# Optimization experiments

Hardware: AMD Instinct MI355X
Metric: run time of the kernel (lower is better)

The kernel has to match this reference:

```python
import jax, jax.numpy as jnp
import numpy as np

DIM = 256; N_HEADS = 8; HEAD_DIM = DIM // N_HEADS
RELU_DIM = 1024; LN_DIM = 512; N_LN = 2; EMB_DIM = 256
VOCAB = 32000; N_CLASSES = 16; B = 8; SEQ = 256
N_ITERS = 12   # fixed-point iterations of the DEQ solve (ITFn2)
EPS = 1e-5     # torch LayerNorm default eps


def sinusoidal_pos_emb(T, d):
    pos = np.arange(T)[:, None].astype(np.float32)
    i = np.arange(d // 2)[None, :].astype(np.float32)
    ang = pos / np.power(10000.0, 2.0 * i / d)
    pe = np.zeros((T, d), np.float32)
    pe[:, 0::2] = np.sin(ang)
    pe[:, 1::2] = np.cos(ang)
    return jnp.asarray(pe)


def setup_inputs() -> dict:
    key = jax.random.key(0)
    ks = jax.random.split(key, 8)
    x = jax.random.randint(ks[0], (B, SEQ), 0, VOCAB)
    seq_lens = jax.random.randint(ks[1], (B,), 1, SEQ + 1)
    emb = jax.random.normal(ks[2], (VOCAB + 1, EMB_DIM), jnp.float32) * EMB_DIM ** -0.5
    emb = emb.at[VOCAB].set(0.0)  # padding_idx row
    cls_token = jax.random.normal(ks[3], (1, 1, EMB_DIM), jnp.float32) * EMB_DIM ** -0.5
    # scaled down vs kaiming so the fixed-point map is contractive (module enforces this via project())
    A = jax.random.normal(ks[4], (RELU_DIM + LN_DIM, RELU_DIM + LN_DIM + DIM + EMB_DIM), jnp.float32) * 0.01
    b = jnp.zeros((RELU_DIM + LN_DIM,), jnp.float32)
    A_qkv = jax.random.normal(ks[5], (3 * DIM, LN_DIM), jnp.float32) * (2.0 / LN_DIM) ** 0.5
    W_cls = jax.random.normal(ks[6], (N_CLASSES, RELU_DIM + LN_DIM + DIM), jnp.float32) * (RELU_DIM + LN_DIM + DIM) ** -0.5
    b_cls = jnp.zeros((N_CLASSES,), jnp.float32)
    return {"x": x, "seq_lens": seq_lens, "emb": emb, "cls_token": cls_token,
            "A": A, "A_qkv": A_qkv, "b": b, "W_cls": W_cls, "b_cls": b_cls}


def reference(x, seq_lens, emb, cls_token, A, A_qkv, b, W_cls, b_cls):
    Bsz, T = x.shape
    Tp = T + 1
    # input injection: embed + sinusoidal pos, then prepend cls token
    u = emb[x] + sinusoidal_pos_emb(T, EMB_DIM)[None]
    u = jnp.concatenate([jnp.broadcast_to(cls_token, (Bsz, 1, EMB_DIM)), u], axis=1)  # (B, T+1, E)
    pos = jnp.arange(Tp)
    src_mask = (seq_lens[:, None] + 1) <= pos[None]  # (B, T+1), True = padded key
    # A_qkv rows ordered (n_heads, 3, head_dim) per scale_by_S rearrange
    Wqkv = A_qkv.reshape(N_HEADS, 3, HEAD_DIM, LN_DIM)
    scale = 1.0 / jnp.sqrt(jnp.asarray(HEAD_DIM, u.dtype))
    neg = jnp.asarray(-1e9, u.dtype)

    def step(z, _):
        # pre-activations for relu + layernorm blocks
        pre = jnp.einsum('btj,ij->bti', jnp.concatenate([z, u], axis=-1), A) + b
        z_r = jax.nn.relu(pre[..., :RELU_DIM])
        zl = pre[..., RELU_DIM:].reshape(Bsz, Tp, N_LN, LN_DIM // N_LN)
        mu = zl.mean(-1, keepdims=True)
        var = zl.var(-1, keepdims=True)
        z_l = ((zl - mu) * jax.lax.rsqrt(var + EPS)).reshape(Bsz, Tp, LN_DIM)
        # multi-head attention driven by the layernorm block
        qkv = jnp.einsum('btj,hmdj->bthmd', z_l, Wqkv)  # (B, T+1, H, 3, hd)
        q, k, v = qkv[..., 0, :], qkv[..., 1, :], qkv[..., 2, :]
        scores = jnp.einsum('bqhd,bkhd->bhqk', q, k) * scale
        scores = jnp.where(src_mask[:, None, None, :], neg, scores)
        attn = jax.nn.softmax(scores, axis=-1)
        z_a = jnp.einsum('bhqk,bkhd->bqhd', attn, v).reshape(Bsz, Tp, DIM)
        return jnp.concatenate([z_r, z_l, z_a], axis=-1), None

    z0 = jnp.zeros((Bsz, Tp, RELU_DIM + LN_DIM + DIM), u.dtype)
    z, _ = jax.lax.scan(step, z0, None, length=N_ITERS)
    # classify from the equilibrium cls-token state
    return z[:, 0] @ W_cls.T + b_cls
```

## Files before the change

kernel.cpp:

```cpp
#include <hip/hip_runtime.h>
#include <hip/hip_bf16.h>
#include <math.h>

#define TP 257
#define ROWS 2056
#define XDIM 2048
#define ZDIM 1792
#define PREDIM 1536
#define QKVDIM 768
#define EMBD 256

using f32x4  = __attribute__((ext_vector_type(4))) float;
using bf16x8 = __attribute__((ext_vector_type(8))) short;

__device__ __forceinline__ ushort f2bf(float f) {
    uint32_t u = __float_as_uint(f);
    return (ushort)((u + 0x7fffu + ((u >> 16) & 1u)) >> 16);
}
__device__ __forceinline__ float bf2f(ushort u) {
    return __uint_as_float(((uint32_t)u) << 16);
}

#define GLD16(g, l) __builtin_amdgcn_global_load_lds( \
    (const __attribute__((address_space(1))) void*)(g), \
    (__attribute__((address_space(3))) void*)(l), 16, 0, 0)

__global__ __launch_bounds__(256) void f2bf_kernel(
    const float* __restrict__ in, ushort* __restrict__ out, int n)
{
    int i = blockIdx.x * 256 + threadIdx.x;
    if (i < n) out[i] = f2bf(in[i]);
}

__global__ __launch_bounds__(256) void build_u_kernel(
    const int* __restrict__ x, const float* __restrict__ emb,
    const float* __restrict__ cls, ushort* __restrict__ xbA, ushort* __restrict__ xbB)
{
    int row = blockIdx.x;
    int e   = threadIdx.x;
    int b = row / TP, t = row % TP;
    float val;
    if (t == 0) {
        val = cls[e];
    } else {
        int tt = t - 1;
        int xi = x[b * 256 + tt];
        float ang = (float)tt * expf(-(float)(e & ~1) * 0.035978672652993f);
        float pe  = (e & 1) ? cosf(ang) : sinf(ang);
        val = emb[(size_t)xi * EMBD + e] + pe;
    }
    ushort bv = f2bf(val);
    xbA[(size_t)row * XDIM + 1792 + e] = bv;
    xbB[(size_t)row * XDIM + 1792 + e] = bv;
}

__global__ __launch_bounds__(256) void gemm_bf16_kernel(
    const ushort* __restrict__ X, int ldx,
    const ushort* __restrict__ W,
    const float* __restrict__ bias,
    float* __restrict__ C, ushort* __restrict__ Cb,
    int ldc, int M, int N, int K)
{
    __shared__ ushort As[128 * 32];
    __shared__ ushort Bs[128 * 32];
    int tid  = threadIdx.x;
    int lane = tid & 63, wv = tid >> 6;
    int wr = wv >> 1, wc = wv & 1;
    int r0 = blockIdx.x * 128, c0 = blockIdx.y * 128;

    f32x4 acc[4][4] = {};

    int srow = wv * 32 + (lane >> 2);
    int skol = (lane & 3) * 8;
    int fk   = (lane >> 4) * 8;

    for (int k0 = 0; k0 < K; k0 += 32) {
        #pragma unroll
        for (int i = 0; i < 2; ++i) {
            int rr = r0 + srow + i * 16;
            if (rr >= M) rr = M - 1;
            const ushort* ga = X + (size_t)rr * ldx + k0 + skol;
            GLD16(ga, &As[(wv * 32 + i * 16) * 32]);
            const ushort* gb = W + (size_t)(c0 + srow + i * 16) * K + k0 + skol;
            GLD16(gb, &Bs[(wv * 32 + i * 16) * 32]);
        }
        __syncthreads();

        bf16x8 a[4], b[4];
        #pragma unroll
        for (int m = 0; m < 4; ++m)
            a[m] = *(const bf16x8*)&As[(wr * 64 + m * 16 + (lane & 15)) * 32 + fk];
        #pragma unroll
        for (int n = 0; n < 4; ++n)
            b[n] = *(const bf16x8*)&Bs[(wc * 64 + n * 16 + (lane & 15)) * 32 + fk];
        #pragma unroll
        for (int m = 0; m < 4; ++m)
            #pragma unroll
            for (int n = 0; n < 4; ++n)
                acc[m][n] = __builtin_amdgcn_mfma_f32_16x16x32_bf16(a[m], b[n], acc[m][n], 0, 0, 0);
        __syncthreads();
    }

    int crow = (lane >> 4) * 4;
    int ccol = lane & 15;
    #pragma unroll
    for (int m = 0; m < 4; ++m) {
        #pragma unroll
        for (int j = 0; j < 4; ++j) {
            int r = r0 + wr * 64 + m * 16 + crow + j;
            if (r < M) {
                #pragma unroll
                for (int n = 0; n < 4; ++n) {
                    int cc = n * 16 + ccol;
                    float vb = bias ? bias[c0 + wc * 64 + cc] : 0.0f;
                    float v = acc[m][n][j] + vb;
                    if (Cb) Cb[(size_t)r * ldc + c0 + wc * 64 + cc] = f2bf(v);
                    else    C [(size_t)r * ldc + c0 + wc * 64 + cc] = v;
                }
            }
        }
    }
}

__global__ __launch_bounds__(256) void relu_ln_kernel(
    const float* __restrict__ pre, ushort* __restrict__ zb)
{
    int row = blockIdx.x;
    int tid = threadIdx.x;
    const float* pr = pre + (size_t)row * PREDIM;
    ushort* zr = zb + (size_t)row * XDIM;

    #pragma unroll
    for (int i = 0; i < 4; ++i) {
        int c = tid + i * 256;
        float v = pr[c];
        zr[c] = f2bf(v > 0.f ? v : 0.f);
    }

    __shared__ float warr[4][2];
    #pragma unroll
    for (int g = 0; g < 2; ++g) {
        float xv = pr[1024 + g * 256 + tid];
        float s = xv, s2 = xv * xv;
        #pragma unroll
        for (int off = 32; off; off >>= 1) {
            s  += __shfl_down(s, off);
            s2 += __shfl_down(s2, off);
        }
        int wave = tid >> 6, lane = tid & 63;
        if (lane == 0) { warr[wave][0] = s; warr[wave][1] = s2; }
        __syncthreads();
        float ts  = warr[0][0] + warr[1][0] + warr[2][0] + warr[3][0];
        float ts2 = warr[0][1] + warr[1][1] + warr[2][1] + warr[3][1];
        float mu  = ts * (1.0f / 256.0f);
        float var = ts2 * (1.0f / 256.0f) - mu * mu;
        float y = (xv - mu) * rsqrtf(var + 1e-5f);
        zr[1024 + g * 256 + tid] = f2bf(y);
        __syncthreads();
    }
}

__global__ __launch_bounds__(256) void attn_kernel(
    const ushort* __restrict__ qkvb, const int* __restrict__ seq_lens,
    ushort* __restrict__ zb)
{
    __shared__ ushort Kl[288 * 40];
    __shared__ ushort VTl[32 * 296];
    __shared__ ushort Pl[4][16 * 40];

    int bh = blockIdx.x;
    int b = bh >> 3, h = bh & 7;
    int kend = seq_lens[b] + 1; if (kend > TP) kend = TP;
    int tid = threadIdx.x;
    const size_t qbase = (size_t)(b * TP) * QKVDIM + h * 96;

    for (int idx = tid; idx < 31 * 32; idx += 256) {
        int row = 257 + (idx >> 5), d = idx & 31;
        Kl[row * 40 + d] = 0;
    }
    for (int idx = tid; idx < 32 * 32; idx += 256) {
        int d = idx >> 5, col = 257 + (idx & 31);
        VTl[d * 296 + col] = 0;
    }
    for (int idx = tid; idx < 257 * 4; idx += 256) {
        int row = idx >> 2, seg = idx & 3;
        *(bf16x8*)&Kl[row * 40 + seg * 8] =
            *(const bf16x8*)&qkvb[qbase + (size_t)row * QKVDIM + 32 + seg * 8];
    }
    for (int idx = tid; idx < 257 * 32; idx += 256) {
        int key = idx >> 5, d = idx & 31;
        VTl[d * 296 + key] = qkvb[qbase + (size_t)key * QKVDIM + 64 + d];
    }
    __syncthreads();

    int wave = tid >> 6, lane = tid & 63;
    int q0 = blockIdx.y * 64 + wave * 16;
    if (q0 > 256) return;
    int qcol = lane & 15, g = lane >> 4;
    int ktmax = (kend + 15) >> 4;
    const float scale = 0.17677669529663687f;

    int qg = q0 + qcol; if (qg > 256) qg = 256;
    bf16x8 aq = *(const bf16x8*)&qkvb[qbase + (size_t)qg * QKVDIM + g * 8];

    f32x4 s[17];
    const f32x4 zz = {};
    #pragma unroll
    for (int kt = 0; kt < 17; ++kt) {
        s[kt] = (f32x4)(-1e30f);
        if (kt < ktmax) {
            bf16x8 bk = *(const bf16x8*)&Kl[(kt * 16 + qcol) * 40 + g * 8];
            f32x4 r = __builtin_amdgcn_mfma_f32_16x16x32_bf16(aq, bk, zz, 0, 0, 0);
            bool kv = (kt * 16 + qcol) < kend;
            #pragma unroll
            for (int j = 0; j < 4; ++j)
                s[kt][j] = kv ? r[j] * scale : -1e30f;
        }
    }

    float m0[4], l0[4];
    #pragma unroll
    for (int j = 0; j < 4; ++j) m0[j] = -3.0e38f;
    #pragma unroll
    for (int kt = 0; kt < 17; ++kt)
        #pragma unroll
        for (int j = 0; j < 4; ++j) m0[j] = fmaxf(m0[j], s[kt][j]);
    #pragma unroll
    for (int j = 0; j < 4; ++j) {
        #pragma unroll
        for (int off = 1; off < 16; off <<= 1)
            m0[j] = fmaxf(m0[j], __shfl_xor(m0[j], off));
        l0[j] = 0.f;
    }
    #pragma unroll
    for (int kt = 0; kt < 17; ++kt)
        #pragma unroll
        for (int j = 0; j < 4; ++j) {
            float p = __expf(s[kt][j] - m0[j]);
            s[kt][j] = p;
            l0[j] += p;
        }
    #pragma unroll
    for (int j = 0; j < 4; ++j) {
        #pragma unroll
        for (int off = 1; off < 16; off <<= 1)
            l0[j] += __shfl_xor(l0[j], off);
        l0[j] = 1.0f / l0[j];
    }
    #pragma unroll
    for (int kt = 0; kt < 17; ++kt)
        #pragma unroll
        for (int j = 0; j < 4; ++j) s[kt][j] *= l0[j];

    f32x4 o[2] = {};
    ushort* Pw = Pl[wave];
    #pragma unroll
    for (int c = 0; c < 9; ++c) {
        if (c * 32 < kend) {
            #pragma unroll
            for (int t = 0; t < 2; ++t)
                #pragma unroll
                for (int j = 0; j < 4; ++j)
                    Pw[(g * 4 + j) * 40 + t * 16 + qcol] = f2bf(s[2 * c + t][j]);
            bf16x8 pa = *(const bf16x8*)&Pw[qcol * 40 + g * 8];
            #pragma unroll
            for (int n = 0; n < 2; ++n) {
                bf16x8 vb = *(const bf16x8*)&VTl[(n * 16 + qcol) * 296 + c * 32 + g * 8];
                o[n] = __builtin_amdgcn_mfma_f32_16x16x32_bf16(pa, vb, o[n], 0, 0, 0);
            }
        }
    }

    #pragma unroll
    for (int n = 0; n < 2; ++n)
        #pragma unroll
        for (int j = 0; j < 4; ++j) {
            int q = q0 + g * 4 + j;
            if (q <= 256)
                zb[(size_t)(b * TP + q) * XDIM + PREDIM + h * 32 + n * 16 + qcol] =
                    f2bf(o[n][j]);
        }
}

__global__ __launch_bounds__(64) void cls_kernel(
    const ushort* __restrict__ zb, const float* __restrict__ W,
    const float* __restrict__ bias, float* __restrict__ out)
{
    int o = blockIdx.x;
    int c = o & 15, b = o >> 4;
    int lane = threadIdx.x;
    const ushort* zr = zb + (size_t)(b * TP) * XDIM;
    const float* wr = W + (size_t)c * ZDIM;
    float s = 0.f;
    for (int j = lane; j < ZDIM; j += 64) s += bf2f(zr[j]) * wr[j];
    #pragma unroll
    for (int off = 32; off; off >>= 1) s += __shfl_down(s, off);
    if (lane == 0) out[b * 16 + c] = s + bias[c];
}

extern "C" void kernel_launch(void* const* d_in, const int* in_sizes, int n_in,
                              void* d_out, int out_size, void* d_ws, size_t ws_size,
                              hipStream_t stream) {
    const int*   x        = (const int*)d_in[0];
    const int*   seq_lens = (const int*)d_in[1];
    const float* emb      = (const float*)d_in[2];
    const float* cls      = (const float*)d_in[3];
    const float* A        = (const float*)d_in[4];
    const float* A_qkv    = (const float*)d_in[5];
    const float* b        = (const float*)d_in[6];
    const float* W_cls    = (const float*)d_in[7];
    const float* b_cls    = (const float*)d_in[8];
    float* out = (float*)d_out;

    ushort* XbA  = (ushort*)d_ws;
    ushort* XbB  = XbA + (size_t)ROWS * XDIM;
    ushort* Ab   = XbB + (size_t)ROWS * XDIM;
    ushort* Aqb  = Ab + (size_t)PREDIM * 2048;
    float*  pre  = (float*)(Aqb + (size_t)QKVDIM * 512);
    ushort* qkvb = (ushort*)pre;

    hipMemsetAsync(XbA, 0, (size_t)ROWS * XDIM * sizeof(ushort), stream);
    f2bf_kernel<<<(PREDIM * 2048 + 255) / 256, 256, 0, stream>>>(A, Ab, PREDIM * 2048);
    f2bf_kernel<<<(QKVDIM * 512 + 255) / 256, 256, 0, stream>>>(A_qkv, Aqb, QKVDIM * 512);
    build_u_kernel<<<ROWS, 256, 0, stream>>>(x, emb, cls, XbA, XbB);

    ushort* cur = XbA;
    ushort* nxt = XbB;
    for (int it = 0; it < 12; ++it) {
        gemm_bf16_kernel<<<dim3(17, 12), 256, 0, stream>>>(
            cur, XDIM, Ab, b, pre, nullptr, PREDIM, ROWS, PREDIM, 2048);
        relu_ln_kernel<<<ROWS, 256, 0, stream>>>(pre, nxt);
        gemm_bf16_kernel<<<dim3(17, 6), 256, 0, stream>>>(
            nxt + 1024, XDIM, Aqb, nullptr, nullptr, qkvb, QKVDIM, ROWS, QKVDIM, 512);
        attn_kernel<<<dim3(64, 5), 256, 0, stream>>>(qkvb, seq_lens, nxt);
        ushort* tmp = cur; cur = nxt; nxt = tmp;
    }
    cls_kernel<<<128, 64, 0, stream>>>(cur, W_cls, b_cls, out);
}
```

Baseline: 1.187 ms.

## Split-K the main DEQ GEMM into two partial buffers summed in relu/LN

The large pre-activation GEMM (17x12 blocks) gets a K-split of two along blockIdx.z when the workspace is big enough, doubling the block count so more of the GPU's compute units are busy. Each split writes its own fp32 partial buffer, the bias is added only by split zero, and the relu/layernorm kernel reads and sums both partials. The relu part of that kernel is also vectorised to float4 loads and ushort4 stores. The cost is an extra fp32 partial buffer written and read back each iteration.

```diff
diff --git a/kernel.cpp b/kernel.cpp
--- a/kernel.cpp
+++ b/kernel.cpp
@@ -59,7 +59,7 @@
     const ushort* __restrict__ W,
     const float* __restrict__ bias,
     float* __restrict__ C, ushort* __restrict__ Cb,
-    int ldc, int M, int N, int K)
+    int ldc, int M, int N, int Ksplit, int Ktotal, size_t splitStride)
 {
     __shared__ ushort As[128 * 32];
     __shared__ ushort Bs[128 * 32];
@@ -67,6 +67,8 @@
     int lane = tid & 63, wv = tid >> 6;
     int wr = wv >> 1, wc = wv & 1;
     int r0 = blockIdx.x * 128, c0 = blockIdx.y * 128;
+    int kbeg = blockIdx.z * Ksplit;
+    int kfin = kbeg + Ksplit;
 
     f32x4 acc[4][4] = {};
 
@@ -74,14 +76,14 @@
     int skol = (lane & 3) * 8;
     int fk   = (lane >> 4) * 8;
 
-    for (int k0 = 0; k0 < K; k0 += 32) {
+    for (int k0 = kbeg; k0 < kfin; k0 += 32) {
         #pragma unroll
         for (int i = 0; i < 2; ++i) {
             int rr = r0 + srow + i * 16;
             if (rr >= M) rr = M - 1;
             const ushort* ga = X + (size_t)rr * ldx + k0 + skol;
             GLD16(ga, &As[(wv * 32 + i * 16) * 32]);
-            const ushort* gb = W + (size_t)(c0 + srow + i * 16) * K + k0 + skol;
+            const ushort* gb = W + (size_t)(c0 + srow + i * 16) * Ktotal + k0 + skol;
             GLD16(gb, &Bs[(wv * 32 + i * 16) * 32]);
         }
         __syncthreads();
@@ -103,6 +105,8 @@
 
     int crow = (lane >> 4) * 4;
     int ccol = lane & 15;
+    float* Cz = C ? C + (size_t)blockIdx.z * splitStride : nullptr;
+    bool addb = (bias != nullptr) && (blockIdx.z == 0);
     #pragma unroll
     for (int m = 0; m < 4; ++m) {
         #pragma unroll
@@ -112,10 +116,10 @@
                 #pragma unroll
                 for (int n = 0; n < 4; ++n) {
                     int cc = n * 16 + ccol;
-                    float vb = bias ? bias[c0 + wc * 64 + cc] : 0.0f;
+                    float vb = addb ? bias[c0 + wc * 64 + cc] : 0.0f;
                     float v = acc[m][n][j] + vb;
                     if (Cb) Cb[(size_t)r * ldc + c0 + wc * 64 + cc] = f2bf(v);
-                    else    C [(size_t)r * ldc + c0 + wc * 64 + cc] = v;
+                    else    Cz[(size_t)r * ldc + c0 + wc * 64 + cc] = v;
                 }
             }
         }
@@ -123,24 +127,32 @@
 }
 
 __global__ __launch_bounds__(256) void relu_ln_kernel(
-    const float* __restrict__ pre, ushort* __restrict__ zb)
+    const float* __restrict__ pre0, const float* __restrict__ pre1,
+    ushort* __restrict__ zb)
 {
     int row = blockIdx.x;
     int tid = threadIdx.x;
-    const float* pr = pre + (size_t)row * PREDIM;
+    const float* p0 = pre0 + (size_t)row * PREDIM;
+    const float* p1 = pre1 ? pre1 + (size_t)row * PREDIM : nullptr;
     ushort* zr = zb + (size_t)row * XDIM;
 
-    #pragma unroll
-    for (int i = 0; i < 4; ++i) {
-        int c = tid + i * 256;
-        float v = pr[c];
-        zr[c] = f2bf(v > 0.f ? v : 0.f);
-    }
+    float4 v = *(const float4*)(p0 + 4 * tid);
+    if (p1) {
+        float4 w = *(const float4*)(p1 + 4 * tid);
+        v.x += w.x; v.y += w.y; v.z += w.z; v.w += w.w;
+    }
+    ushort4 o;
+    o.x = f2bf(v.x > 0.f ? v.x : 0.f);
+    o.y = f2bf(v.y > 0.f ? v.y : 0.f);
+    o.z = f2bf(v.z > 0.f ? v.z : 0.f);
+    o.w = f2bf(v.w > 0.f ? v.w : 0.f);
+    *(ushort4*)(zr + 4 * tid) = o;
 
     __shared__ float warr[4][2];
     #pragma unroll
     for (int g = 0; g < 2; ++g) {
-        float xv = pr[1024 + g * 256 + tid];
+        int c = 1024 + g * 256 + tid;
+        float xv = p0[c] + (p1 ? p1[c] : 0.f);
         float s = xv, s2 = xv * xv;
         #pragma unroll
         for (int off = 32; off; off >>= 1) {
@@ -155,7 +167,7 @@
         float mu  = ts * (1.0f / 256.0f);
         float var = ts2 * (1.0f / 256.0f) - mu * mu;
         float y = (xv - mu) * rsqrtf(var + 1e-5f);
-        zr[1024 + g * 256 + tid] = f2bf(y);
+        zr[c] = f2bf(y);
         __syncthreads();
     }
 }
@@ -316,8 +328,12 @@
     ushort* XbB  = XbA + (size_t)ROWS * XDIM;
     ushort* Ab   = XbB + (size_t)ROWS * XDIM;
     ushort* Aqb  = Ab + (size_t)PREDIM * 2048;
-    float*  pre  = (float*)(Aqb + (size_t)QKVDIM * 512);
-    ushort* qkvb = (ushort*)pre;
+    float*  pre0 = (float*)(Aqb + (size_t)QKVDIM * 512);
+    float*  pre1 = pre0 + (size_t)ROWS * PREDIM;
+    ushort* qkvb = (ushort*)pre0;
+
+    size_t need2 = (size_t)((char*)(pre1 + (size_t)ROWS * PREDIM) - (char*)d_ws);
+    int nsplit = (ws_size >= need2) ? 2 : 1;
 
     hipMemsetAsync(XbA, 0, (size_t)ROWS * XDIM * sizeof(ushort), stream);
     f2bf_kernel<<<(PREDIM * 2048 + 255) / 256, 256, 0, stream>>>(A, Ab, PREDIM * 2048);
@@ -327,11 +343,14 @@
     ushort* cur = XbA;
     ushort* nxt = XbB;
     for (int it = 0; it < 12; ++it) {
-        gemm_bf16_kernel<<<dim3(17, 12), 256, 0, stream>>>(
-            cur, XDIM, Ab, b, pre, nullptr, PREDIM, ROWS, PREDIM, 2048);
-        relu_ln_kernel<<<ROWS, 256, 0, stream>>>(pre, nxt);
-        gemm_bf16_kernel<<<dim3(17, 6), 256, 0, stream>>>(
-            nxt + 1024, XDIM, Aqb, nullptr, nullptr, qkvb, QKVDIM, ROWS, QKVDIM, 512);
+        gemm_bf16_kernel<<<dim3(17, 12, nsplit), 256, 0, stream>>>(
+            cur, XDIM, Ab, b, pre0, nullptr, PREDIM, ROWS, PREDIM,
+            2048 / nsplit, 2048, (size_t)ROWS * PREDIM);
+        relu_ln_kernel<<<ROWS, 256, 0, stream>>>(
+            pre0, nsplit == 2 ? pre1 : nullptr, nxt);
+        gemm_bf16_kernel<<<dim3(17, 6, 1), 256, 0, stream>>>(
+            nxt + 1024, XDIM, Aqb, nullptr, nullptr, qkvb, QKVDIM, ROWS, QKVDIM,
+            512, 512, 0);
         attn_kernel<<<dim3(64, 5), 256, 0, stream>>>(qkvb, seq_lens, nxt);
         ushort* tmp = cur; cur = nxt; nxt = tmp;
     }
```

After: 1.014 ms. -14.6%, faster.
